# Kernel tuning notes

Measured on AMD Instinct MI355X. Metric: run time of the kernel, lower is better.

Reference implementation:

```python
import jax, jax.numpy as jnp
import numpy as np

N_NODES = 100000
N_EDGES = 1600000
NFEAT = 128
NHID = 128
NCLASS = 40


def setup_inputs() -> dict:
    key = jax.random.key(0)
    ks = jax.random.split(key, 12)
    s = 0.05
    return {
        "x": jax.random.normal(ks[0], (N_NODES, NFEAT), jnp.float32),
        "edge_index": jax.random.randint(ks[1], (2, N_EDGES), 0, N_NODES, jnp.int64),
        "W_pre": jax.random.normal(ks[2], (NHID, NFEAT), jnp.float32) * s,
        "b_pre": jax.random.normal(ks[3], (NHID,), jnp.float32) * s,
        "Wl0": jax.random.normal(ks[4], (NHID, NHID), jnp.float32) * s,
        "bl0": jax.random.normal(ks[5], (NHID,), jnp.float32) * s,
        "Wr0": jax.random.normal(ks[6], (NHID, NHID), jnp.float32) * s,
        "Wl1": jax.random.normal(ks[7], (NHID, NHID), jnp.float32) * s,
        "bl1": jax.random.normal(ks[8], (NHID,), jnp.float32) * s,
        "Wr1": jax.random.normal(ks[9], (NHID, NHID), jnp.float32) * s,
        "W_post": jax.random.normal(ks[10], (NCLASS, NHID), jnp.float32) * s,
        "b_post": jax.random.normal(ks[11], (NCLASS,), jnp.float32) * s,
    }


def _sage_conv(x, src, dst, Wl, bl, Wr):
    # PyG SAGEConv (mean aggr): out = lin_l(mean_{j->i} x_j) + lin_r(x_i)
    n = x.shape[0]
    agg = jax.ops.segment_sum(x[src], dst, num_segments=n)  # [N, H]
    cnt = jax.ops.segment_sum(jnp.ones((src.shape[0],), x.dtype), dst, num_segments=n)
    agg = agg / jnp.maximum(cnt, 1.0)[:, None]
    return agg @ Wl.T + bl + x @ Wr.T


def reference(x, edge_index, W_pre, b_pre, Wl0, bl0, Wr0, Wl1, bl1, Wr1, W_post, b_post):
    src, dst = edge_index[0], edge_index[1]
    h = x @ W_pre.T + b_pre  # pre-linear
    h = jax.nn.relu(_sage_conv(h, src, dst, Wl0, bl0, Wr0))  # dropout identity (eval)
    h = jax.nn.relu(_sage_conv(h, src, dst, Wl1, bl1, Wr1))
    logits = h @ W_post.T + b_post
    return jax.nn.log_softmax(logits, axis=1)
```

## Files before the change

### kernel.cpp

```cpp
#include <hip/hip_runtime.h>
#include <hip/hip_bf16.h>
#include <math.h>

#define N_NODES 100000
#define N_EDGES 1600000
#define NF 128
#define NC 40

#define NB 256
#define NPB 391
#define CAP 8192
#define PART_BLOCKS 512
#define PART_E ((N_EDGES + PART_BLOCKS - 1) / PART_BLOCKS)

#define WB_ELEMS (5 * 16384 + 48 * 128)

typedef __attribute__((ext_vector_type(8))) short short8v;
typedef __attribute__((ext_vector_type(4))) float f32x4;
typedef __attribute__((ext_vector_type(2))) float f32x2;
typedef unsigned short ushort_t;

__device__ inline float bflo(unsigned v) { union { unsigned u; float f; } x; x.u = v << 16; return x.f; }
__device__ inline float bfhi(unsigned v) { union { unsigned u; float f; } x; x.u = v & 0xffff0000u; return x.f; }
__device__ inline ushort_t f2bf(float f) {
    __hip_bfloat16 h = __float2bfloat16(f);
    return __builtin_bit_cast(ushort_t, h);
}

__device__ inline void acc_fp8x8p(uint2 v, f32x2& a0, f32x2& a1, f32x2& a2, f32x2& a3) {
    a0 += __builtin_amdgcn_cvt_pk_f32_fp8((int)v.x, false);
    a1 += __builtin_amdgcn_cvt_pk_f32_fp8((int)v.x, true);
    a2 += __builtin_amdgcn_cvt_pk_f32_fp8((int)v.y, false);
    a3 += __builtin_amdgcn_cvt_pk_f32_fp8((int)v.y, true);
}


__global__ __launch_bounds__(256) void k_part(const int* __restrict__ src,
                                              const int* __restrict__ dst,
                                              unsigned* __restrict__ bcur,
                                              uint2* __restrict__ pairs) {
    __shared__ unsigned cnt[NB];
    __shared__ unsigned curs[NB];
    const int t = threadIdx.x;
    cnt[t] = 0;
    __syncthreads();
    const int e0 = blockIdx.x * PART_E;
    int e1 = e0 + PART_E; if (e1 > N_EDGES) e1 = N_EDGES;
    for (int e = e0 + t; e < e1; e += 256)
        atomicAdd(&cnt[dst[e] / NPB], 1u);
    __syncthreads();
    unsigned c = cnt[t];
    curs[t] = c ? atomicAdd(&bcur[t], c) : 0u;
    __syncthreads();
    for (int e = e0 + t; e < e1; e += 256) {
        int d = dst[e];
        int s = src[e];
        int b = d / NPB;
        unsigned p = atomicAdd(&curs[b], 1u);
        if (p < CAP) pairs[(size_t)b * CAP + p] = make_uint2((unsigned)d, (unsigned)s);
    }
}


__global__ void k_bscan(const unsigned* __restrict__ bcur,
                        unsigned* __restrict__ bbase,
                        unsigned* __restrict__ rowptr) {
    __shared__ unsigned s[NB];
    const int t = threadIdx.x;
    unsigned v = bcur[t];
    s[t] = v; __syncthreads();
    for (int off = 1; off < NB; off <<= 1) {
        unsigned u = (t >= off) ? s[t - off] : 0;
        __syncthreads();
        s[t] += u;
        __syncthreads();
    }
    bbase[t] = s[t] - v;
    if (t == NB - 1) rowptr[N_NODES] = s[NB - 1];
}


__global__ __launch_bounds__(256) void k_bucket(const uint2* __restrict__ pairs,
                                                const unsigned* __restrict__ bcur,
                                                const unsigned* __restrict__ bbase,
                                                unsigned* __restrict__ rowptr,
                                                unsigned* __restrict__ srcs) {
    __shared__ unsigned s[512];
    const int t = threadIdx.x;
    const int b = blockIdx.x;
    unsigned cnt = bcur[b]; if (cnt > CAP) cnt = CAP;
    const unsigned base = bbase[b];
    const int n0 = b * NPB;
    int nn = N_NODES - n0; if (nn > NPB) nn = NPB;
    const uint2* pp = pairs + (size_t)b * CAP;

    s[t] = 0; s[t + 256] = 0;
    __syncthreads();
    for (unsigned i = t; i < cnt; i += 256)
        atomicAdd(&s[pp[i].x - n0], 1u);
    __syncthreads();
    unsigned d0 = s[t], d1 = s[t + 256];
    for (int off = 1; off < 512; off <<= 1) {
        unsigned u0 = (t >= off) ? s[t - off] : 0;
        unsigned u1 = (t + 256 >= off) ? s[t + 256 - off] : 0;
        __syncthreads();
        s[t] += u0; s[t + 256] += u1;
        __syncthreads();
    }
    unsigned ex0 = base + s[t] - d0;
    unsigned ex1 = base + s[t + 256] - d1;
    __syncthreads();
    s[t] = ex0; s[t + 256] = ex1;
    if (t < nn) rowptr[n0 + t] = ex0;
    if (t + 256 < nn) rowptr[n0 + t + 256] = ex1;
    __syncthreads();
    for (unsigned i = t; i < cnt; i += 256) {
        uint2 e = pp[i];
        unsigned p = atomicAdd(&s[e.x - n0], 1u);
        srcs[p] = e.y;
    }
}


__global__ void k_castw(const float* __restrict__ w0, const float* __restrict__ w1,
                        const float* __restrict__ w2, const float* __restrict__ w3,
                        const float* __restrict__ w4, const float* __restrict__ wp,
                        ushort_t* __restrict__ out) {
    int i = blockIdx.x * 256 + threadIdx.x;
    if (i < 5 * 16384) {
        int m = i >> 14, j = i & 16383;
        const float* s = (m == 0) ? w0 : (m == 1) ? w1 : (m == 2) ? w2 : (m == 3) ? w3 : w4;
        out[i] = f2bf(s[j]);
    } else if (i < WB_ELEMS) {
        int j = i - 5 * 16384;
        int row = j >> 7, col = j & 127;
        out[i] = (row < NC) ? f2bf(wp[row * NF + col]) : (ushort_t)0;
    }
}


__global__ __launch_bounds__(256) void k_aggregate8(const uint2* __restrict__ h64,
                                                    const unsigned* __restrict__ rowptr,
                                                    const unsigned* __restrict__ srcs,
                                                    ushort_t* __restrict__ agg) {
    int wave = threadIdx.x >> 6;
    int lane = threadIdx.x & 63;
    int node = blockIdx.x * 4 + wave;
    if (node >= N_NODES) return;
    const int slot = lane >> 4;
    const int d = lane & 15;
    unsigned beg = rowptr[node], end = rowptr[node + 1];
    f32x2 a0 = {0.f, 0.f}, a1 = {0.f, 0.f}, a2 = {0.f, 0.f}, a3 = {0.f, 0.f};
    unsigned i = beg;
    for (; i + 16 <= end; i += 16) {
        unsigned s0 = srcs[i + slot];
        unsigned s1 = srcs[i + 4 + slot];
        unsigned s2 = srcs[i + 8 + slot];
        unsigned s3 = srcs[i + 12 + slot];
        uint2 v0 = h64[(size_t)s0 * 16 + d];
        uint2 v1 = h64[(size_t)s1 * 16 + d];
        uint2 v2 = h64[(size_t)s2 * 16 + d];
        uint2 v3 = h64[(size_t)s3 * 16 + d];
        acc_fp8x8p(v0, a0, a1, a2, a3);
        acc_fp8x8p(v1, a0, a1, a2, a3);
        acc_fp8x8p(v2, a0, a1, a2, a3);
        acc_fp8x8p(v3, a0, a1, a2, a3);
    }
    if (i + 8 <= end) {
        unsigned s0 = srcs[i + slot];
        unsigned s1 = srcs[i + 4 + slot];
        uint2 v0 = h64[(size_t)s0 * 16 + d];
        uint2 v1 = h64[(size_t)s1 * 16 + d];
        acc_fp8x8p(v0, a0, a1, a2, a3);
        acc_fp8x8p(v1, a0, a1, a2, a3);
        i += 8;
    }
    if (i + 4 <= end) {
        unsigned s0 = srcs[i + slot];
        uint2 v0 = h64[(size_t)s0 * 16 + d];
        acc_fp8x8p(v0, a0, a1, a2, a3);
        i += 4;
    }
    if (i + slot < end) {
        unsigned s0 = srcs[i + slot];
        uint2 v0 = h64[(size_t)s0 * 16 + d];
        acc_fp8x8p(v0, a0, a1, a2, a3);
    }
    float r[8] = {a0.x, a0.y, a1.x, a1.y, a2.x, a2.y, a3.x, a3.y};
#pragma unroll
    for (int j = 0; j < 8; ++j) {
        r[j] += __shfl_xor(r[j], 16, 64);
        r[j] += __shfl_xor(r[j], 32, 64);
    }
    if (slot == 0) {
        float sc = 1.f / fmaxf((float)(end - beg), 1.f);
        uint4 o;
        o.x = ((unsigned)f2bf(r[1] * sc) << 16) | (unsigned)f2bf(r[0] * sc);
        o.y = ((unsigned)f2bf(r[3] * sc) << 16) | (unsigned)f2bf(r[2] * sc);
        o.z = ((unsigned)f2bf(r[5] * sc) << 16) | (unsigned)f2bf(r[4] * sc);
        o.w = ((unsigned)f2bf(r[7] * sc) << 16) | (unsigned)f2bf(r[6] * sc);
        ((uint4*)(agg + (size_t)node * NF))[d] = o;
    }
}


template <int SRC_F32, int HAS2, int POST>
__global__ __launch_bounds__(512) void k_gemm(const void* __restrict__ A1v,
                                              const ushort_t* __restrict__ A2,
                                              const ushort_t* __restrict__ W1,
                                              const ushort_t* __restrict__ W2,
                                              const float* __restrict__ bias,
                                              ushort_t* __restrict__ out,
                                              unsigned char* __restrict__ out8,
                                              const ushort_t* __restrict__ Wp,
                                              const float* __restrict__ bp,
                                              float* __restrict__ outf) {
    constexpr int LDSZ = (HAS2 ? 65536 : 32768) + (POST ? 12288 : 0);
    __shared__ char ldsc[LDSZ];
    const int t = threadIdx.x;
    const int lane = t & 63;
    const int wv = t >> 6;
    const int r0 = blockIdx.x * 128 + wv * 16;
    const int lr = lane & 15;
    const int kg = lane >> 4;

    {
        const int nchunk1 = 128 * 16;
        for (int c = t; c < nchunk1; c += 512) {
            int row = c >> 4, s16 = c & 15;
            uint4 v = ((const uint4*)(W1 + (size_t)row * NF))[s16];
            *(uint4*)(&ldsc[row * 256 + ((s16 * 16) ^ ((row & 7) << 4))]) = v;
        }
        if (HAS2) {
            for (int c = t; c < nchunk1; c += 512) {
                int row = c >> 4, s16 = c & 15;
                uint4 v = ((const uint4*)(W2 + (size_t)row * NF))[s16];
                int lrow = 128 + row;
                *(uint4*)(&ldsc[lrow * 256 + ((s16 * 16) ^ ((lrow & 7) << 4))]) = v;
            }
        }
        if (POST) {
            for (int c = t; c < 48 * 16; c += 512) {
                int row = c >> 4, s16 = c & 15;
                uint4 v = ((const uint4*)(Wp + (size_t)row * NF))[s16];
                int lrow = 256 + row;
                *(uint4*)(&ldsc[lrow * 256 + ((s16 * 16) ^ ((lrow & 7) << 4))]) = v;
            }
        }
    }

    int arow = r0 + lr;
    if (arow >= N_NODES) arow = N_NODES - 1;
    short8v af1[4], af2[4];
    if (SRC_F32) {
        const float* x = (const float*)A1v;
#pragma unroll
        for (int ks = 0; ks < 4; ++ks) {
            const float4* xp = (const float4*)(x + (size_t)arow * NF + ks * 32 + kg * 8);
            float4 f0 = xp[0], f1 = xp[1];
            short8v v;
            v[0] = (short)f2bf(f0.x); v[1] = (short)f2bf(f0.y);
            v[2] = (short)f2bf(f0.z); v[3] = (short)f2bf(f0.w);
            v[4] = (short)f2bf(f1.x); v[5] = (short)f2bf(f1.y);
            v[6] = (short)f2bf(f1.z); v[7] = (short)f2bf(f1.w);
            af1[ks] = v;
        }
    } else {
        const ushort_t* A1 = (const ushort_t*)A1v;
        const short8v* a1p = (const short8v*)(A1 + (size_t)arow * NF + kg * 8);
#pragma unroll
        for (int ks = 0; ks < 4; ++ks) af1[ks] = a1p[ks * 4];
    }
    if (HAS2) {
        const short8v* a2p = (const short8v*)(A2 + (size_t)arow * NF + kg * 8);
#pragma unroll
        for (int ks = 0; ks < 4; ++ks) af2[ks] = a2p[ks * 4];
    }
    __syncthreads();

    f32x4 acc[8];
#pragma unroll
    for (int ct = 0; ct < 8; ++ct) acc[ct] = (f32x4){0.f, 0.f, 0.f, 0.f};
#pragma unroll
    for (int ct = 0; ct < 8; ++ct) {
#pragma unroll
        for (int ks = 0; ks < 4; ++ks) {
            int row = ct * 16 + lr;
            short8v b = *(const short8v*)(&ldsc[row * 256 + ((ks * 64 + kg * 16) ^ ((row & 7) << 4))]);
            acc[ct] = __builtin_amdgcn_mfma_f32_16x16x32_bf16(af1[ks], b, acc[ct], 0, 0, 0);
        }
        if (HAS2) {
#pragma unroll
            for (int ks = 0; ks < 4; ++ks) {
                int row = 128 + ct * 16 + lr;
                short8v b = *(const short8v*)(&ldsc[row * 256 + ((ks * 64 + kg * 16) ^ ((row & 7) << 4))]);
                acc[ct] = __builtin_amdgcn_mfma_f32_16x16x32_bf16(af2[ks], b, acc[ct], 0, 0, 0);
            }
        }
    }

    if (POST == 0) {
        __syncthreads();
#pragma unroll
        for (int ct = 0; ct < 8; ++ct) {
            float bv = bias[ct * 16 + lr];
#pragma unroll
            for (int r = 0; r < 4; ++r) {
                float v = acc[ct][r] + bv;
                if (!SRC_F32) v = fmaxf(v, 0.f);
                int row = wv * 16 + kg * 4 + r;
                int boff = (ct * 32 + lr * 2) ^ ((row & 7) << 4);
                *(ushort_t*)(&ldsc[row * 256 + boff]) = f2bf(v);
            }
        }
        __syncthreads();
        {
            const int row = t >> 2;
            const int seg = t & 3;
            const int grow = blockIdx.x * 128 + row;
            uint4 vv[4];
#pragma unroll
            for (int k = 0; k < 4; ++k) {
                int s16 = seg * 4 + k;
                vv[k] = *(const uint4*)(&ldsc[row * 256 + ((s16 * 16) ^ ((row & 7) << 4))]);
            }
            if (grow < N_NODES) {
                uint4* op = (uint4*)(out + (size_t)grow * NF);
#pragma unroll
                for (int k = 0; k < 4; ++k) op[seg * 4 + k] = vv[k];
                const unsigned* u = (const unsigned*)vv;
                unsigned f8[8];
#pragma unroll
                for (int k = 0; k < 8; ++k) {
                    int p0 = __builtin_amdgcn_cvt_pk_fp8_f32(bflo(u[2 * k]), bfhi(u[2 * k]), 0, false);
                    f8[k] = (unsigned)__builtin_amdgcn_cvt_pk_fp8_f32(bflo(u[2 * k + 1]), bfhi(u[2 * k + 1]), p0, true);
                }
                uint4* o8 = (uint4*)(out8 + (size_t)grow * NF + seg * 32);
                o8[0] = make_uint4(f8[0], f8[1], f8[2], f8[3]);
                o8[1] = make_uint4(f8[4], f8[5], f8[6], f8[7]);
            }
        }
    } else {
        __syncthreads();
#pragma unroll
        for (int ct = 0; ct < 8; ++ct) {
            float bv = bias[ct * 16 + lr];
#pragma unroll
            for (int r = 0; r < 4; ++r) {
                float v = fmaxf(acc[ct][r] + bv, 0.f);
                int row = wv * 16 + kg * 4 + r;
                int boff = (ct * 32 + lr * 2) ^ ((row & 7) << 4);
                *(ushort_t*)(&ldsc[row * 256 + boff]) = f2bf(v);
            }
        }
        __syncthreads();

        const int lrow = wv * 16 + lr;
        short8v afp[4];
#pragma unroll
        for (int ks = 0; ks < 4; ++ks) {
            int boff = (ks * 64 + kg * 16) ^ ((lrow & 7) << 4);
            afp[ks] = *(const short8v*)(&ldsc[lrow * 256 + boff]);
        }
        f32x4 accp[3];
#pragma unroll
        for (int cp = 0; cp < 3; ++cp) accp[cp] = (f32x4){0.f, 0.f, 0.f, 0.f};
#pragma unroll
        for (int cp = 0; cp < 3; ++cp) {
#pragma unroll
            for (int ks = 0; ks < 4; ++ks) {
                int row = 256 + cp * 16 + lr;
                short8v b = *(const short8v*)(&ldsc[row * 256 + ((ks * 64 + kg * 16) ^ ((row & 7) << 4))]);
                accp[cp] = __builtin_amdgcn_mfma_f32_16x16x32_bf16(afp[ks], b, accp[cp], 0, 0, 0);
            }
        }
        float bp0 = bp[lr];
        float bp1 = bp[16 + lr];
        float bp2 = (lr < 8) ? bp[32 + lr] : 0.f;
#pragma unroll
        for (int r = 0; r < 4; ++r) {
            float v0 = accp[0][r] + bp0;
            float v1 = accp[1][r] + bp1;
            float v2 = (lr < 8) ? (accp[2][r] + bp2) : -INFINITY;
            float m = fmaxf(fmaxf(v0, v1), v2);
#pragma unroll
            for (int off = 8; off; off >>= 1) m = fmaxf(m, __shfl_xor(m, off, 16));
            float s = expf(v0 - m) + expf(v1 - m) + ((lr < 8) ? expf(v2 - m) : 0.f);
#pragma unroll
            for (int off = 8; off; off >>= 1) s += __shfl_xor(s, off, 16);
            float ls = m + logf(s);
            int node = r0 + kg * 4 + r;
            if (node < N_NODES) {
                outf[(size_t)node * NC + lr] = v0 - ls;
                outf[(size_t)node * NC + 16 + lr] = v1 - ls;
                if (lr < 8) outf[(size_t)node * NC + 32 + lr] = v2 - ls;
            }
        }
    }
}


extern "C" void kernel_launch(void* const* d_in, const int* in_sizes, int n_in,
                              void* d_out, int out_size, void* d_ws, size_t ws_size,
                              hipStream_t stream) {
    const float* x      = (const float*)d_in[0];
    const int*   ei     = (const int*)d_in[1];
    const float* W_pre  = (const float*)d_in[2];
    const float* b_pre  = (const float*)d_in[3];
    const float* Wl0    = (const float*)d_in[4];
    const float* bl0    = (const float*)d_in[5];
    const float* Wr0    = (const float*)d_in[6];
    const float* Wl1    = (const float*)d_in[7];
    const float* bl1    = (const float*)d_in[8];
    const float* Wr1    = (const float*)d_in[9];
    const float* W_post = (const float*)d_in[10];
    const float* b_post = (const float*)d_in[11];
    const int* src = ei;
    const int* dst = ei + N_EDGES;

    const size_t act_bytes = (size_t)N_NODES * NF * 2;
    const size_t act8_bytes = (size_t)N_NODES * NF;
    char* w = (char*)d_ws;
    ushort_t* h0   = (ushort_t*)w; w += act_bytes;
    ushort_t* h1   = (ushort_t*)w; w += act_bytes;
    ushort_t* aggb = (ushort_t*)w; w += act_bytes;
    unsigned char* h0f8 = (unsigned char*)w; w += act8_bytes;
    unsigned char* h1f8 = (unsigned char*)w; w += act8_bytes;
    ushort_t* wb   = (ushort_t*)w; w += (size_t)WB_ELEMS * 2;
    unsigned* rowptr = (unsigned*)w; w += (size_t)(N_NODES + 32) * 4;
    unsigned* bcur   = (unsigned*)w; w += 256 * 4;
    unsigned* bbase  = (unsigned*)w; w += 256 * 4;
    unsigned* srcs   = (unsigned*)w; w += (size_t)N_EDGES * 4;
    uint2* pairs     = (uint2*)w;   w += (size_t)NB * CAP * 8;

    ushort_t* wb_pre  = wb;
    ushort_t* wb_l0   = wb + 16384;
    ushort_t* wb_r0   = wb + 2 * 16384;
    ushort_t* wb_l1   = wb + 3 * 16384;
    ushort_t* wb_r1   = wb + 4 * 16384;
    ushort_t* wb_post = wb + 5 * 16384;

    float* outp = (float*)d_out;

    hipMemsetAsync(bcur, 0, NB * 4, stream);
    k_part<<<PART_BLOCKS, 256, 0, stream>>>(src, dst, bcur, pairs);
    k_bscan<<<1, NB, 0, stream>>>(bcur, bbase, rowptr);
    k_bucket<<<NB, 256, 0, stream>>>(pairs, bcur, bbase, rowptr, srcs);

    k_castw<<<(WB_ELEMS + 255) / 256, 256, 0, stream>>>(W_pre, Wl0, Wr0, Wl1, Wr1, W_post, wb);

    const int gemm_grid = (N_NODES + 127) / 128;
    const int node_grid = (N_NODES + 3) / 4;

    k_gemm<1, 0, 0><<<gemm_grid, 512, 0, stream>>>(x, nullptr, wb_pre, nullptr, b_pre,
                                                   h0, h0f8, nullptr, nullptr, nullptr);
    k_aggregate8<<<node_grid, 256, 0, stream>>>((const uint2*)h0f8, rowptr, srcs, aggb);
    k_gemm<0, 1, 0><<<gemm_grid, 512, 0, stream>>>(aggb, h0, wb_l0, wb_r0, bl0,
                                                   h1, h1f8, nullptr, nullptr, nullptr);
    k_aggregate8<<<node_grid, 256, 0, stream>>>((const uint2*)h1f8, rowptr, srcs, aggb);
    k_gemm<0, 1, 1><<<gemm_grid, 512, 0, stream>>>(aggb, h1, wb_l1, wb_r1, bl1,
                                                   nullptr, nullptr, wb_post, b_post, outp);
}
```

Before: 224.1 us.

## Process two row tiles per block in the first two GEMMs with prefetch overlap

Adds a k_gemm2 kernel that handles two 128-row tiles per block, so the weight matrices are staged into LDS once for two tiles instead of once per tile. The A-fragments of the second tile are loaded before the first tile's writeback, overlapping global loads with the writeback. The writeback is split so half the threads store the bf16 output and the other half store the fp8 copy. The block uses more LDS and registers, and the grid is halved, which reduces parallelism for the pre-linear and first SAGE layer GEMMs.

Result: faster. 216.9 us (-3.2%).

```diff
diff --git a/kernel.cpp b/kernel.cpp
--- a/kernel.cpp
+++ b/kernel.cpp
@@ -32,6 +32,15 @@
     a1 += __builtin_amdgcn_cvt_pk_f32_fp8((int)v.x, true);
     a2 += __builtin_amdgcn_cvt_pk_f32_fp8((int)v.y, false);
     a3 += __builtin_amdgcn_cvt_pk_f32_fp8((int)v.y, true);
+}
+
+__device__ inline short8v cvt_f32x8_bf16(float4 f0, float4 f1) {
+    short8v v;
+    v[0] = (short)f2bf(f0.x); v[1] = (short)f2bf(f0.y);
+    v[2] = (short)f2bf(f0.z); v[3] = (short)f2bf(f0.w);
+    v[4] = (short)f2bf(f1.x); v[5] = (short)f2bf(f1.y);
+    v[6] = (short)f2bf(f1.z); v[7] = (short)f2bf(f1.w);
+    return v;
 }
 
 
@@ -60,7 +69,6 @@
         if (p < CAP) pairs[(size_t)b * CAP + p] = make_uint2((unsigned)d, (unsigned)s);
     }
 }
-
 
 __global__ void k_bscan(const unsigned* __restrict__ bcur,
                         unsigned* __restrict__ bbase,
@@ -78,7 +86,6 @@
     bbase[t] = s[t] - v;
     if (t == NB - 1) rowptr[N_NODES] = s[NB - 1];
 }
-
 
 __global__ __launch_bounds__(256) void k_bucket(const uint2* __restrict__ pairs,
                                                 const unsigned* __restrict__ bcur,
@@ -204,6 +211,180 @@
 }
 
 
+template <int SRC_F32, int HAS2>
+__global__ __launch_bounds__(512, 4) void k_gemm2(const void* __restrict__ A1v,
+                                                  const ushort_t* __restrict__ A2,
+                                                  const ushort_t* __restrict__ W1,
+                                                  const ushort_t* __restrict__ W2,
+                                                  const float* __restrict__ bias,
+                                                  ushort_t* __restrict__ out,
+                                                  unsigned char* __restrict__ out8) {
+    constexpr int WLDS = HAS2 ? 65536 : 32768;
+    __shared__ char ldsc[WLDS + 16384];
+    char* wbl = ldsc + WLDS;
+    const int t = threadIdx.x;
+    const int lane = t & 63;
+    const int wv = t >> 6;
+    const int lr = lane & 15;
+    const int kg = lane >> 4;
+    const int tile0 = blockIdx.x * 2;
+
+    {
+        const int n1 = 128 * 16;
+        for (int c = t; c < n1; c += 512) {
+            int row = c >> 4, s16 = c & 15;
+            uint4 v = ((const uint4*)(W1 + (size_t)row * NF))[s16];
+            *(uint4*)(&ldsc[row * 256 + ((s16 * 16) ^ ((row & 7) << 4))]) = v;
+        }
+        if (HAS2) {
+            for (int c = t; c < n1; c += 512) {
+                int row = c >> 4, s16 = c & 15;
+                uint4 v = ((const uint4*)(W2 + (size_t)row * NF))[s16];
+                int lrow = 128 + row;
+                *(uint4*)(&ldsc[lrow * 256 + ((s16 * 16) ^ ((lrow & 7) << 4))]) = v;
+            }
+        }
+    }
+
+    float bv[8];
+#pragma unroll
+    for (int ct = 0; ct < 8; ++ct) bv[ct] = bias[ct * 16 + lr];
+
+    auto do_mfma = [&](short8v (&a1)[4], short8v (&a2)[4], f32x4 (&ac)[8]) {
+#pragma unroll
+        for (int ct = 0; ct < 8; ++ct) ac[ct] = (f32x4){0.f, 0.f, 0.f, 0.f};
+#pragma unroll
+        for (int ct = 0; ct < 8; ++ct) {
+#pragma unroll
+            for (int ks = 0; ks < 4; ++ks) {
+                int row = ct * 16 + lr;
+                short8v b = *(const short8v*)(&ldsc[row * 256 + ((ks * 64 + kg * 16) ^ ((row & 7) << 4))]);
+                ac[ct] = __builtin_amdgcn_mfma_f32_16x16x32_bf16(a1[ks], b, ac[ct], 0, 0, 0);
+            }
+            if (HAS2) {
+#pragma unroll
+                for (int ks = 0; ks < 4; ++ks) {
+                    int row = 128 + ct * 16 + lr;
+                    short8v b = *(const short8v*)(&ldsc[row * 256 + ((ks * 64 + kg * 16) ^ ((row & 7) << 4))]);
+                    ac[ct] = __builtin_amdgcn_mfma_f32_16x16x32_bf16(a2[ks], b, ac[ct], 0, 0, 0);
+                }
+            }
+        }
+    };
+
+    auto writeback = [&](int tile, f32x4 (&ac)[8]) {
+#pragma unroll
+        for (int pass = 0; pass < 2; ++pass) {
+            __syncthreads();
+            if ((wv >> 2) == pass) {
+#pragma unroll
+                for (int ct = 0; ct < 8; ++ct) {
+#pragma unroll
+                    for (int r = 0; r < 4; ++r) {
+                        float v = ac[ct][r] + bv[ct];
+                        if (!SRC_F32) v = fmaxf(v, 0.f);
+                        int row = (wv & 3) * 16 + kg * 4 + r;
+                        int boff = (ct * 32 + lr * 2) ^ ((row & 7) << 4);
+                        *(ushort_t*)(&wbl[row * 256 + boff]) = f2bf(v);
+                    }
+                }
+            }
+            __syncthreads();
+            const int u = t & 255;
+            const int row = u >> 2, seg = u & 3;
+            const int grow = tile * 128 + pass * 64 + row;
+            uint4 vv[4];
+#pragma unroll
+            for (int k = 0; k < 4; ++k) {
+                int s16 = seg * 4 + k;
+                vv[k] = *(const uint4*)(&wbl[row * 256 + ((s16 * 16) ^ ((row & 7) << 4))]);
+            }
+            if (grow < N_NODES) {
+                if (t < 256) {
+                    uint4* op = (uint4*)(out + (size_t)grow * NF);
+#pragma unroll
+                    for (int k = 0; k < 4; ++k) op[seg * 4 + k] = vv[k];
+                } else {
+                    const unsigned* uu = (const unsigned*)vv;
+                    unsigned f8[8];
+#pragma unroll
+                    for (int k = 0; k < 8; ++k) {
+                        int p0 = __builtin_amdgcn_cvt_pk_fp8_f32(bflo(uu[2 * k]), bfhi(uu[2 * k]), 0, false);
+                        f8[k] = (unsigned)__builtin_amdgcn_cvt_pk_fp8_f32(bflo(uu[2 * k + 1]), bfhi(uu[2 * k + 1]), p0, true);
+                    }
+                    uint4* o8 = (uint4*)(out8 + (size_t)grow * NF + seg * 32);
+                    o8[0] = make_uint4(f8[0], f8[1], f8[2], f8[3]);
+                    o8[1] = make_uint4(f8[4], f8[5], f8[6], f8[7]);
+                }
+            }
+        }
+    };
+
+    short8v afA1[4], afA2[4];
+    {
+        int arow = tile0 * 128 + wv * 16 + lr;
+        if (arow >= N_NODES) arow = N_NODES - 1;
+        if (SRC_F32) {
+            const float* x = (const float*)A1v;
+#pragma unroll
+            for (int ks = 0; ks < 4; ++ks) {
+                const float4* xp = (const float4*)(x + (size_t)arow * NF + ks * 32 + kg * 8);
+                afA1[ks] = cvt_f32x8_bf16(xp[0], xp[1]);
+            }
+        } else {
+            const short8v* p = (const short8v*)((const ushort_t*)A1v + (size_t)arow * NF + kg * 8);
+#pragma unroll
+            for (int ks = 0; ks < 4; ++ks) afA1[ks] = p[ks * 4];
+        }
+        if (HAS2) {
+            const short8v* p2 = (const short8v*)(A2 + (size_t)arow * NF + kg * 8);
+#pragma unroll
+            for (int ks = 0; ks < 4; ++ks) afA2[ks] = p2[ks * 4];
+        }
+    }
+    __syncthreads();
+
+    f32x4 acc[8];
+    do_mfma(afA1, afA2, acc);
+
+    short8v afB1[4], afB2[4];
+    float4 rawB[8];
+    {
+        int arow = (tile0 + 1) * 128 + wv * 16 + lr;
+        if (arow >= N_NODES) arow = N_NODES - 1;
+        if (SRC_F32) {
+            const float* x = (const float*)A1v;
+#pragma unroll
+            for (int ks = 0; ks < 4; ++ks) {
+                const float4* xp = (const float4*)(x + (size_t)arow * NF + ks * 32 + kg * 8);
+                rawB[2 * ks] = xp[0];
+                rawB[2 * ks + 1] = xp[1];
+            }
+        } else {
+            const short8v* p = (const short8v*)((const ushort_t*)A1v + (size_t)arow * NF + kg * 8);
+#pragma unroll
+            for (int ks = 0; ks < 4; ++ks) afB1[ks] = p[ks * 4];
+        }
+        if (HAS2) {
+            const short8v* p2 = (const short8v*)(A2 + (size_t)arow * NF + kg * 8);
+#pragma unroll
+            for (int ks = 0; ks < 4; ++ks) afB2[ks] = p2[ks * 4];
+        }
+    }
+
+    writeback(tile0, acc);
+
+    if (SRC_F32) {
+#pragma unroll
+        for (int ks = 0; ks < 4; ++ks)
+            afB1[ks] = cvt_f32x8_bf16(rawB[2 * ks], rawB[2 * ks + 1]);
+    }
+
+    do_mfma(afB1, afB2, acc);
+    writeback(tile0 + 1, acc);
+}
+
+
 template <int SRC_F32, int HAS2, int POST>
 __global__ __launch_bounds__(512) void k_gemm(const void* __restrict__ A1v,
                                               const ushort_t* __restrict__ A2,
@@ -257,13 +438,7 @@
 #pragma unroll
         for (int ks = 0; ks < 4; ++ks) {
             const float4* xp = (const float4*)(x + (size_t)arow * NF + ks * 32 + kg * 8);
-            float4 f0 = xp[0], f1 = xp[1];
-            short8v v;
-            v[0] = (short)f2bf(f0.x); v[1] = (short)f2bf(f0.y);
-            v[2] = (short)f2bf(f0.z); v[3] = (short)f2bf(f0.w);
-            v[4] = (short)f2bf(f1.x); v[5] = (short)f2bf(f1.y);
-            v[6] = (short)f2bf(f1.z); v[7] = (short)f2bf(f1.w);
-            af1[ks] = v;
+            af1[ks] = cvt_f32x8_bf16(xp[0], xp[1]);
         }
     } else {
         const ushort_t* A1 = (const ushort_t*)A1v;
@@ -299,55 +474,14 @@
         }
     }
 
-    if (POST == 0) {
+    {
         __syncthreads();
 #pragma unroll
         for (int ct = 0; ct < 8; ++ct) {
-            float bv = bias[ct * 16 + lr];
+            float bvv = bias[ct * 16 + lr];
 #pragma unroll
             for (int r = 0; r < 4; ++r) {
-                float v = acc[ct][r] + bv;
-                if (!SRC_F32) v = fmaxf(v, 0.f);
-                int row = wv * 16 + kg * 4 + r;
-                int boff = (ct * 32 + lr * 2) ^ ((row & 7) << 4);
-                *(ushort_t*)(&ldsc[row * 256 + boff]) = f2bf(v);
-            }
-        }
-        __syncthreads();
-        {
-            const int row = t >> 2;
-            const int seg = t & 3;
-            const int grow = blockIdx.x * 128 + row;
-            uint4 vv[4];
-#pragma unroll
-            for (int k = 0; k < 4; ++k) {
-                int s16 = seg * 4 + k;
-                vv[k] = *(const uint4*)(&ldsc[row * 256 + ((s16 * 16) ^ ((row & 7) << 4))]);
-            }
-            if (grow < N_NODES) {
-                uint4* op = (uint4*)(out + (size_t)grow * NF);
-#pragma unroll
-                for (int k = 0; k < 4; ++k) op[seg * 4 + k] = vv[k];
-                const unsigned* u = (const unsigned*)vv;
-                unsigned f8[8];
-#pragma unroll
-                for (int k = 0; k < 8; ++k) {
-                    int p0 = __builtin_amdgcn_cvt_pk_fp8_f32(bflo(u[2 * k]), bfhi(u[2 * k]), 0, false);
-                    f8[k] = (unsigned)__builtin_amdgcn_cvt_pk_fp8_f32(bflo(u[2 * k + 1]), bfhi(u[2 * k + 1]), p0, true);
-                }
-                uint4* o8 = (uint4*)(out8 + (size_t)grow * NF + seg * 32);
-                o8[0] = make_uint4(f8[0], f8[1], f8[2], f8[3]);
-                o8[1] = make_uint4(f8[4], f8[5], f8[6], f8[7]);
-            }
-        }
-    } else {
-        __syncthreads();
-#pragma unroll
-        for (int ct = 0; ct < 8; ++ct) {
-            float bv = bias[ct * 16 + lr];
-#pragma unroll
-            for (int r = 0; r < 4; ++r) {
-                float v = fmaxf(acc[ct][r] + bv, 0.f);
+                float v = fmaxf(acc[ct][r] + bvv, 0.f);
                 int row = wv * 16 + kg * 4 + r;
                 int boff = (ct * 32 + lr * 2) ^ ((row & 7) << 4);
                 *(ushort_t*)(&ldsc[row * 256 + boff]) = f2bf(v);
@@ -449,15 +583,14 @@
 
     k_castw<<<(WB_ELEMS + 255) / 256, 256, 0, stream>>>(W_pre, Wl0, Wr0, Wl1, Wr1, W_post, wb);
 
+    const int g2 = (N_NODES + 255) / 256;
     const int gemm_grid = (N_NODES + 127) / 128;
     const int node_grid = (N_NODES + 3) / 4;
 
-    k_gemm<1, 0, 0><<<gemm_grid, 512, 0, stream>>>(x, nullptr, wb_pre, nullptr, b_pre,
-                                                   h0, h0f8, nullptr, nullptr, nullptr);
+    k_gemm2<1, 0><<<g2, 512, 0, stream>>>(x, nullptr, wb_pre, nullptr, b_pre, h0, h0f8);
     k_aggregate8<<<node_grid, 256, 0, stream>>>((const uint2*)h0f8, rowptr, srcs, aggb);
-    k_gemm<0, 1, 0><<<gemm_grid, 512, 0, stream>>>(aggb, h0, wb_l0, wb_r0, bl0,
-                                                   h1, h1f8, nullptr, nullptr, nullptr);
+    k_gemm2<0, 1><<<g2, 512, 0, stream>>>(aggb, h0, wb_l0, wb_r0, bl0, h1, h1f8);
     k_aggregate8<<<node_grid, 256, 0, stream>>>((const uint2*)h1f8, rowptr, srcs, aggb);
-    k_gemm<0, 1, 1><<<gemm_grid, 512, 0, stream>>>(aggb, h1, wb_l1, wb_r1, bl1,
-                                                   nullptr, nullptr, wb_post, b_post, outp);
-}
+    k_gemm<0, 1, 1><<<gemm_grid, 512, 0, stream>>>(aggb, h1, wb_l1, wb_r1, bl1, nullptr, nullptr,
+                                                   wb_post, b_post, outp);
+}
```
